# Kernel optimization log

Hardware: AMD Instinct MI355X
Metric: run time of the kernel (lower is better)

## Reference

```python
import jax, jax.numpy as jnp
import numpy as np

IN_FEATURES = 4096
OUT_FEATURES = 16384
TOKENS = 8192  # batch 2 * seq 4096, flattened


def setup_inputs() -> dict:
    key = jax.random.key(0)
    k_x, k_w, k_s, k_b = jax.random.split(key, 4)
    x = jax.random.normal(k_x, (TOKENS, IN_FEATURES), dtype=jnp.float32)
    # ternary weights in {-1, 0, +1}, stored as low-precision ints
    weight_ternary = jax.random.randint(k_w, (OUT_FEATURES, IN_FEATURES), 0, 3, dtype=jnp.int32) - 1
    weight_scale = jax.random.uniform(k_s, (1,), dtype=jnp.float32) + 0.5
    bias = jax.random.normal(k_b, (OUT_FEATURES,), dtype=jnp.float32)
    return {"x": x, "weight_ternary": weight_ternary, "weight_scale": weight_scale, "bias": bias}


def reference(x, weight_ternary, weight_scale, bias):
    # forward: out = x @ (ternary.float() * scale).T + bias  (F.linear)
    w_float = weight_ternary.astype(jnp.float32) * weight_scale  # [O, I]
    out = jnp.einsum('ti,oi->to', x, w_float) + bias  # [T, O]
    return out
```

## Files before the change

### kernel.cpp

```cpp
#include <hip/hip_runtime.h>
#include <stdint.h>

#define TOKENS 8192
#define IN_F   4096
#define OUT_F  16384

#define BM 256
#define BN 256
#define BK 128
#define NT (IN_F / BK)

typedef __attribute__((ext_vector_type(4))) float f32x4;
typedef __attribute__((ext_vector_type(4))) int i32x4;


__device__ __forceinline__ int pack4(int a, int b, int c, int d) {
  return (a & 0xff) | ((b & 0xff) << 8) | ((c & 0xff) << 16) | ((d & 0xff) << 24);
}

__global__ void convert_w_i8(const int* __restrict__ w,
                             int8_t* __restrict__ wq, int n16) {
  int stride = gridDim.x * blockDim.x;
  for (int i = blockIdx.x * blockDim.x + threadIdx.x; i < n16; i += stride) {
    i32x4 o;
#pragma unroll
    for (int j = 0; j < 4; ++j) {
      i32x4 a = ((const i32x4*)w)[(size_t)i * 4 + j];
      o[j] = pack4(a.x, a.y, a.z, a.w);
    }
    ((i32x4*)wq)[i] = o;
  }
}

__global__ void convert_x_i8(const float* __restrict__ x,
                             int8_t* __restrict__ xq,
                             float* __restrict__ xs) {
  const int t = blockIdx.x;
  const int tid = threadIdx.x;
  const float* xr = x + (size_t)t * IN_F;

  f32x4 v[4];
  float m = 0.f;
#pragma unroll
  for (int i = 0; i < 4; ++i) {
    v[i] = ((const f32x4*)xr)[tid * 4 + i];
    m = fmaxf(m, fmaxf(fmaxf(fabsf(v[i].x), fabsf(v[i].y)),
                       fmaxf(fabsf(v[i].z), fabsf(v[i].w))));
  }
#pragma unroll
  for (int off = 32; off; off >>= 1) m = fmaxf(m, __shfl_xor(m, off));
  __shared__ float sm[4];
  if ((tid & 63) == 0) sm[tid >> 6] = m;
  __syncthreads();
  m = fmaxf(fmaxf(sm[0], sm[1]), fmaxf(sm[2], sm[3]));

  const float inv = (m > 0.f) ? (127.f / m) : 0.f;
  if (tid == 0) xs[t] = m / 127.f;

  i32x4 o;
#pragma unroll
  for (int i = 0; i < 4; ++i) {
    o[i] = pack4(__float2int_rn(v[i].x * inv), __float2int_rn(v[i].y * inv),
                 __float2int_rn(v[i].z * inv), __float2int_rn(v[i].w * inv));
  }
  ((i32x4*)(xq + (size_t)t * IN_F))[tid] = o;
}


__device__ __forceinline__ void async_lds_16B(const int8_t* g, int8_t* l) {
  __builtin_amdgcn_global_load_lds(
      reinterpret_cast<const __attribute__((address_space(1))) unsigned int*>(
          reinterpret_cast<uintptr_t>(g)),
      reinterpret_cast<__attribute__((address_space(3))) unsigned int*>(
          reinterpret_cast<uintptr_t>(l)),
      16, 0, 0);
}

__global__ __launch_bounds__(512, 2)
void ternary_gemm_i8(const int8_t* __restrict__ A,
                     const int8_t* __restrict__ B,
                     const float* __restrict__ xs,
                     const float* __restrict__ scale_p,
                     const float* __restrict__ bias,
                     float* __restrict__ C) {
  __shared__ __attribute__((aligned(16))) int8_t lds[2][2][BM * BK];

  const int nbn = OUT_F / BN;
  const int cpx = gridDim.x >> 3;
  const int bid = blockIdx.x;
  const int swz = (bid & 7) * cpx + (bid >> 3);
  const int bm = swz / nbn;
  const int bn = swz % nbn;

  const int tid  = threadIdx.x;
  const int lane = tid & 63;
  const int wid  = tid >> 6;
  const int wr   = wid >> 2;
  const int wc   = wid & 3;

  const int r = lane & 15;
  const int g = lane >> 4;
  const int swzr = (r & 7) * 16;

  const int8_t* Ag = A + (size_t)bm * BM * IN_F;
  const int8_t* Bg = B + (size_t)bn * BN * IN_F;

  const int s_rowoff = lane >> 3;
  const int s_colb   = ((lane & 7) ^ (lane >> 3)) * 16;

  auto stage = [&](int8_t* ldsTile, const int8_t* gTile, int half, int kt) {
#pragma unroll
    for (int i = 0; i < 2; ++i) {
      const int rbase = half * 128 + wid * 16 + i * 8;
      const int8_t* src =
          gTile + (size_t)(rbase + s_rowoff) * IN_F + kt * BK + s_colb;
      async_lds_16B(src, ldsTile + rbase * BK);
    }
  };

  i32x4 acc[8][4];
#pragma unroll
  for (int m = 0; m < 8; ++m)
#pragma unroll
    for (int n = 0; n < 4; ++n) acc[m][n] = i32x4{0, 0, 0, 0};

  stage(&lds[0][1][0], Bg, 0, 0);
  stage(&lds[0][1][0], Bg, 1, 0);
  stage(&lds[0][0][0], Ag, 0, 0);
  stage(&lds[0][0][0], Ag, 1, 0);
  stage(&lds[1][1][0], Bg, 0, 1);
  stage(&lds[1][1][0], Bg, 1, 1);
  stage(&lds[1][0][0], Ag, 0, 1);
  asm volatile("s_waitcnt vmcnt(6)" ::: "memory");
  __builtin_amdgcn_s_barrier();

  for (int t = 0; t < NT; ++t) {
    const int cur = t & 1;
    const int8_t* Ab = &lds[cur][0][0];
    const int8_t* Bb = &lds[cur][1][0];
    int8_t* Abw = &lds[cur][0][0];
    int8_t* Bbw = &lds[cur][1][0];
    int8_t* An  = &lds[cur ^ 1][0][0];

    i32x4 bfr[4][2];
#pragma unroll
    for (int n = 0; n < 4; ++n)
#pragma unroll
      for (int ks = 0; ks < 2; ++ks)
        bfr[n][ks] = *(const i32x4*)(Bb + (wc * 64 + n * 16 + r) * BK +
                                     ((ks * 64 + g * 16) ^ swzr));
    i32x4 a0[2][2];
#pragma unroll
    for (int m = 0; m < 2; ++m)
#pragma unroll
      for (int ks = 0; ks < 2; ++ks)
        a0[m][ks] = *(const i32x4*)(Ab + (wr * 128 + m * 16 + r) * BK +
                                    ((ks * 64 + g * 16) ^ swzr));
    if (t + 1 < NT) stage(An, Ag, 1, t + 1);
    __builtin_amdgcn_s_barrier();
    asm volatile("s_waitcnt lgkmcnt(0)" ::: "memory");
    __builtin_amdgcn_s_setprio(1);
#pragma unroll
    for (int ks = 0; ks < 2; ++ks)
#pragma unroll
      for (int m = 0; m < 2; ++m)
#pragma unroll
        for (int n = 0; n < 4; ++n)
          acc[m][n] = __builtin_amdgcn_mfma_i32_16x16x64_i8(
              a0[m][ks], bfr[n][ks], acc[m][n], 0, 0, 0);
    __builtin_amdgcn_s_setprio(0);
    __builtin_amdgcn_s_barrier();

    i32x4 a1[2][2];
#pragma unroll
    for (int m = 0; m < 2; ++m)
#pragma unroll
      for (int ks = 0; ks < 2; ++ks)
        a1[m][ks] = *(const i32x4*)(Ab + (wr * 128 + (2 + m) * 16 + r) * BK +
                                    ((ks * 64 + g * 16) ^ swzr));
    if (t + 2 < NT) stage(Bbw, Bg, 0, t + 2);
    __builtin_amdgcn_s_barrier();
    asm volatile("s_waitcnt lgkmcnt(0)" ::: "memory");
    __builtin_amdgcn_s_setprio(1);
#pragma unroll
    for (int ks = 0; ks < 2; ++ks)
#pragma unroll
      for (int m = 0; m < 2; ++m)
#pragma unroll
        for (int n = 0; n < 4; ++n)
          acc[2 + m][n] = __builtin_amdgcn_mfma_i32_16x16x64_i8(
              a1[m][ks], bfr[n][ks], acc[2 + m][n], 0, 0, 0);
    __builtin_amdgcn_s_setprio(0);
    __builtin_amdgcn_s_barrier();

    i32x4 a2[2][2], a3[2][2];
#pragma unroll
    for (int m = 0; m < 2; ++m)
#pragma unroll
      for (int ks = 0; ks < 2; ++ks) {
        a2[m][ks] = *(const i32x4*)(Ab + (wr * 128 + (4 + m) * 16 + r) * BK +
                                    ((ks * 64 + g * 16) ^ swzr));
        a3[m][ks] = *(const i32x4*)(Ab + (wr * 128 + (6 + m) * 16 + r) * BK +
                                    ((ks * 64 + g * 16) ^ swzr));
      }
    if (t + 2 < NT) stage(Bbw, Bg, 1, t + 2);
    __builtin_amdgcn_s_barrier();
    asm volatile("s_waitcnt lgkmcnt(0)" ::: "memory");
    __builtin_amdgcn_s_setprio(1);
#pragma unroll
    for (int ks = 0; ks < 2; ++ks)
#pragma unroll
      for (int m = 0; m < 2; ++m)
#pragma unroll
        for (int n = 0; n < 4; ++n)
          acc[4 + m][n] = __builtin_amdgcn_mfma_i32_16x16x64_i8(
              a2[m][ks], bfr[n][ks], acc[4 + m][n], 0, 0, 0);
    __builtin_amdgcn_s_setprio(0);
    __builtin_amdgcn_s_barrier();

    if (t + 2 < NT) {
      stage(Abw, Ag, 0, t + 2);
      asm volatile("s_waitcnt vmcnt(6)" ::: "memory");
    } else {
      asm volatile("s_waitcnt vmcnt(0)" ::: "memory");
    }
    __builtin_amdgcn_s_barrier();
    asm volatile("s_waitcnt lgkmcnt(0)" ::: "memory");
    __builtin_amdgcn_s_setprio(1);
#pragma unroll
    for (int ks = 0; ks < 2; ++ks)
#pragma unroll
      for (int m = 0; m < 2; ++m)
#pragma unroll
        for (int n = 0; n < 4; ++n)
          acc[6 + m][n] = __builtin_amdgcn_mfma_i32_16x16x64_i8(
              a3[m][ks], bfr[n][ks], acc[6 + m][n], 0, 0, 0);
    __builtin_amdgcn_s_setprio(0);
    __builtin_amdgcn_s_barrier();
  }

  const float s = scale_p[0];
  const int row0 = bm * BM + wr * 128;
  const int col0 = bn * BN + wc * 64;
  float bv[4];
#pragma unroll
  for (int n = 0; n < 4; ++n) bv[n] = bias[col0 + n * 16 + r];
#pragma unroll
  for (int m = 0; m < 8; ++m) {
#pragma unroll
    for (int j = 0; j < 4; ++j) {
      const int row = row0 + m * 16 + g * 4 + j;
      const float sx = xs[row] * s;
#pragma unroll
      for (int n = 0; n < 4; ++n) {
        const int col = col0 + n * 16 + r;
        C[(size_t)row * OUT_F + col] = (float)acc[m][n][j] * sx + bv[n];
      }
    }
  }
}


__global__ void fallback_kernel(const float* __restrict__ x,
                                const int* __restrict__ w,
                                const float* __restrict__ scale_p,
                                const float* __restrict__ bias,
                                float* __restrict__ out) {
  size_t idx = (size_t)blockIdx.x * 256 + threadIdx.x;
  int t = (int)(idx / OUT_F);
  int o = (int)(idx % OUT_F);
  const float* xr = x + (size_t)t * IN_F;
  const int* wr = w + (size_t)o * IN_F;
  float acc = 0.f;
  for (int k = 0; k < IN_F; ++k) acc += xr[k] * (float)wr[k];
  out[idx] = acc * scale_p[0] + bias[o];
}


extern "C" void kernel_launch(void* const* d_in, const int* in_sizes, int n_in,
                              void* d_out, int out_size, void* d_ws, size_t ws_size,
                              hipStream_t stream) {
  const float* x     = (const float*)d_in[0];
  const int*   w     = (const int*)d_in[1];
  const float* scale = (const float*)d_in[2];
  const float* bias  = (const float*)d_in[3];
  float* out = (float*)d_out;

  const size_t wq_bytes = (size_t)OUT_F * IN_F;
  const size_t xq_bytes = (size_t)TOKENS * IN_F;
  const size_t xs_bytes = (size_t)TOKENS * sizeof(float);

  if (ws_size >= wq_bytes + xq_bytes + xs_bytes) {
    int8_t* wq = (int8_t*)d_ws;
    int8_t* xq = (int8_t*)((char*)d_ws + wq_bytes);
    float*  xs = (float*)((char*)d_ws + wq_bytes + xq_bytes);

    convert_w_i8<<<2048, 256, 0, stream>>>(w, wq, (OUT_F * IN_F) / 16);
    convert_x_i8<<<TOKENS, 256, 0, stream>>>(x, xq, xs);

    dim3 grid((TOKENS / BM) * (OUT_F / BN));
    ternary_gemm_i8<<<grid, 512, 0, stream>>>(xq, wq, xs, scale, bias, out);
  } else {
    size_t total = (size_t)TOKENS * OUT_F;
    fallback_kernel<<<(unsigned)(total / 256), 256, 0, stream>>>(x, w, scale, bias, out);
  }
}
```

Baseline: 624.5 us.

## Software-pipeline LDS fragment loads one phase ahead of MFMA blocks

Hoists the B and first A fragment reads out of each iteration so they are loaded for the next K-tile at the end of the current one. Each later A fragment is read from LDS right after the previous MFMA block, so the reads overlap the matrix math. This removes the explicit lgkmcnt(0) waits and one barrier per phase. It keeps more fragments live in registers, and it reads the next tile's LDS data before the final barrier, which risks reading before other waves' global-to-LDS loads have landed.

```diff
diff --git a/kernel.cpp b/kernel.cpp
--- a/kernel.cpp
+++ b/kernel.cpp
@@ -134,31 +134,30 @@
   asm volatile("s_waitcnt vmcnt(6)" ::: "memory");
   __builtin_amdgcn_s_barrier();
 
+  i32x4 bfr[4][2];
+  i32x4 a0[2][2], a1[2][2], a2[2][2], a3[2][2];
+#pragma unroll
+  for (int n = 0; n < 4; ++n)
+#pragma unroll
+    for (int ks = 0; ks < 2; ++ks)
+      bfr[n][ks] = *(const i32x4*)(&lds[0][1][0] + (wc * 64 + n * 16 + r) * BK +
+                                   ((ks * 64 + g * 16) ^ swzr));
+#pragma unroll
+  for (int m = 0; m < 2; ++m)
+#pragma unroll
+    for (int ks = 0; ks < 2; ++ks)
+      a0[m][ks] = *(const i32x4*)(&lds[0][0][0] + (wr * 128 + m * 16 + r) * BK +
+                                  ((ks * 64 + g * 16) ^ swzr));
+
   for (int t = 0; t < NT; ++t) {
     const int cur = t & 1;
     const int8_t* Ab = &lds[cur][0][0];
-    const int8_t* Bb = &lds[cur][1][0];
     int8_t* Abw = &lds[cur][0][0];
     int8_t* Bbw = &lds[cur][1][0];
     int8_t* An  = &lds[cur ^ 1][0][0];
-
-    i32x4 bfr[4][2];
-#pragma unroll
-    for (int n = 0; n < 4; ++n)
-#pragma unroll
-      for (int ks = 0; ks < 2; ++ks)
-        bfr[n][ks] = *(const i32x4*)(Bb + (wc * 64 + n * 16 + r) * BK +
-                                     ((ks * 64 + g * 16) ^ swzr));
-    i32x4 a0[2][2];
-#pragma unroll
-    for (int m = 0; m < 2; ++m)
-#pragma unroll
-      for (int ks = 0; ks < 2; ++ks)
-        a0[m][ks] = *(const i32x4*)(Ab + (wr * 128 + m * 16 + r) * BK +
-                                    ((ks * 64 + g * 16) ^ swzr));
-    if (t + 1 < NT) stage(An, Ag, 1, t + 1);
-    __builtin_amdgcn_s_barrier();
-    asm volatile("s_waitcnt lgkmcnt(0)" ::: "memory");
+    const int8_t* AbN = &lds[cur ^ 1][0][0];
+    const int8_t* BbN = &lds[cur ^ 1][1][0];
+
     __builtin_amdgcn_s_setprio(1);
 #pragma unroll
     for (int ks = 0; ks < 2; ++ks)
@@ -169,18 +168,15 @@
           acc[m][n] = __builtin_amdgcn_mfma_i32_16x16x64_i8(
               a0[m][ks], bfr[n][ks], acc[m][n], 0, 0, 0);
     __builtin_amdgcn_s_setprio(0);
-    __builtin_amdgcn_s_barrier();
-
-    i32x4 a1[2][2];
 #pragma unroll
     for (int m = 0; m < 2; ++m)
 #pragma unroll
       for (int ks = 0; ks < 2; ++ks)
         a1[m][ks] = *(const i32x4*)(Ab + (wr * 128 + (2 + m) * 16 + r) * BK +
                                     ((ks * 64 + g * 16) ^ swzr));
-    if (t + 2 < NT) stage(Bbw, Bg, 0, t + 2);
+    if (t + 1 < NT) stage(An, Ag, 1, t + 1);
     __builtin_amdgcn_s_barrier();
-    asm volatile("s_waitcnt lgkmcnt(0)" ::: "memory");
+
     __builtin_amdgcn_s_setprio(1);
 #pragma unroll
     for (int ks = 0; ks < 2; ++ks)
@@ -191,21 +187,15 @@
           acc[2 + m][n] = __builtin_amdgcn_mfma_i32_16x16x64_i8(
               a1[m][ks], bfr[n][ks], acc[2 + m][n], 0, 0, 0);
     __builtin_amdgcn_s_setprio(0);
-    __builtin_amdgcn_s_barrier();
-
-    i32x4 a2[2][2], a3[2][2];
 #pragma unroll
     for (int m = 0; m < 2; ++m)
 #pragma unroll
-      for (int ks = 0; ks < 2; ++ks) {
+      for (int ks = 0; ks < 2; ++ks)
         a2[m][ks] = *(const i32x4*)(Ab + (wr * 128 + (4 + m) * 16 + r) * BK +
                                     ((ks * 64 + g * 16) ^ swzr));
-        a3[m][ks] = *(const i32x4*)(Ab + (wr * 128 + (6 + m) * 16 + r) * BK +
-                                    ((ks * 64 + g * 16) ^ swzr));
-      }
-    if (t + 2 < NT) stage(Bbw, Bg, 1, t + 2);
+    if (t + 2 < NT) stage(Bbw, Bg, 0, t + 2);
     __builtin_amdgcn_s_barrier();
-    asm volatile("s_waitcnt lgkmcnt(0)" ::: "memory");
+
     __builtin_amdgcn_s_setprio(1);
 #pragma unroll
     for (int ks = 0; ks < 2; ++ks)
@@ -216,26 +206,45 @@
           acc[4 + m][n] = __builtin_amdgcn_mfma_i32_16x16x64_i8(
               a2[m][ks], bfr[n][ks], acc[4 + m][n], 0, 0, 0);
     __builtin_amdgcn_s_setprio(0);
+#pragma unroll
+    for (int m = 0; m < 2; ++m)
+#pragma unroll
+      for (int ks = 0; ks < 2; ++ks)
+        a3[m][ks] = *(const i32x4*)(Ab + (wr * 128 + (6 + m) * 16 + r) * BK +
+                                    ((ks * 64 + g * 16) ^ swzr));
+    if (t + 2 < NT) stage(Bbw, Bg, 1, t + 2);
     __builtin_amdgcn_s_barrier();
 
+    __builtin_amdgcn_s_setprio(1);
+#pragma unroll
+    for (int ks = 0; ks < 2; ++ks)
+#pragma unroll
+      for (int m = 0; m < 2; ++m)
+#pragma unroll
+        for (int n = 0; n < 4; ++n)
+          acc[6 + m][n] = __builtin_amdgcn_mfma_i32_16x16x64_i8(
+              a3[m][ks], bfr[n][ks], acc[6 + m][n], 0, 0, 0);
+    __builtin_amdgcn_s_setprio(0);
     if (t + 2 < NT) {
       stage(Abw, Ag, 0, t + 2);
       asm volatile("s_waitcnt vmcnt(6)" ::: "memory");
     } else {
       asm volatile("s_waitcnt vmcnt(0)" ::: "memory");
     }
-    __builtin_amdgcn_s_barrier();
-    asm volatile("s_waitcnt lgkmcnt(0)" ::: "memory");
-    __builtin_amdgcn_s_setprio(1);
-#pragma unroll
-    for (int ks = 0; ks < 2; ++ks)
-#pragma unroll
-      for (int m = 0; m < 2; ++m)
-#pragma unroll
-        for (int n = 0; n < 4; ++n)
-          acc[6 + m][n] = __builtin_amdgcn_mfma_i32_16x16x64_i8(
-              a3[m][ks], bfr[n][ks], acc[6 + m][n], 0, 0, 0);
-    __builtin_amdgcn_s_setprio(0);
+    if (t + 1 < NT) {
+#pragma unroll
+      for (int n = 0; n < 4; ++n)
+#pragma unroll
+        for (int ks = 0; ks < 2; ++ks)
+          bfr[n][ks] = *(const i32x4*)(BbN + (wc * 64 + n * 16 + r) * BK +
+                                       ((ks * 64 + g * 16) ^ swzr));
+#pragma unroll
+      for (int m = 0; m < 2; ++m)
+#pragma unroll
+        for (int ks = 0; ks < 2; ++ks)
+          a0[m][ks] = *(const i32x4*)(AbN + (wr * 128 + m * 16 + r) * BK +
+                                      ((ks * 64 + g * 16) ^ swzr));
+    }
     __builtin_amdgcn_s_barrier();
   }
 
```

After: 615.3 us. No clear change (-1.5%).
